# Kernel tuning notes

Hardware: AMD Instinct MI355X
Metric: run time of the kernel (lower is better)

The kernel has to match this reference:

```python
import jax, jax.numpy as jnp
import numpy as np

ALPHA = 13
B_POOL = 1.0
KERNEL = 2
STRIDE = 2
PADDING = 0


def _poly_eval(x, c):
    # Horner evaluation of sum_k c[k] * x**k (same math as power-basis sum)
    acc = jnp.zeros_like(x) + c[-1]
    for k in range(c.shape[0] - 2, -1, -1):
        acc = acc * x + c[k]
    return acc


def _sgn_approx(x, coeff_stages):
    # composed polynomial approximation of sign(x); B_relu = 1.0 so x/B == x
    for c in coeff_stages:
        x = _poly_eval(x, c)
    return x


def _max_approx(a, b, coeff_stages):
    d = a - b
    return (a + b + d * _sgn_approx(d, coeff_stages)) / 2.0


def setup_inputs() -> dict:
    key = jax.random.key(0)
    k1, k2, k3 = jax.random.split(key, 3)
    x = jax.random.uniform(k1, (32, 64, 112, 112), dtype=jnp.float32,
                           minval=-0.9, maxval=0.9)
    coeffs0 = 0.3 * jax.random.normal(k2, (8,), dtype=jnp.float32)
    coeffs1 = 0.3 * jax.random.normal(k3, (8,), dtype=jnp.float32)
    return {"x": x, "coeffs0": coeffs0, "coeffs1": coeffs1}


def reference(x, coeffs0, coeffs1):
    coeff_stages = (coeffs0, coeffs1)
    # zero padding (padding = 0 here, kept for generality)
    xp = jnp.pad(x, ((0, 0), (0, 0), (PADDING, PADDING), (PADDING, PADDING)))
    N, C, W, H = xp.shape
    i_num = (W - KERNEL) // STRIDE + 1  # 56
    j_num = (H - KERNEL) // STRIDE + 1  # 56
    # strided window extraction (im2col of the 2x2 pooling windows)
    ext = [xp[:, :, i:i + STRIDE * i_num:STRIDE, j:j + STRIDE * j_num:STRIDE]
           for i in range(KERNEL) for j in range(KERNEL)]
    # scale into the valid range of the sign approximation
    scaling_factor = (1.0 - 4.0 * 0.5 ** ALPHA) / (B_POOL * 2.0)
    ext = [e * scaling_factor + 0.5 for e in ext]
    # binary max tree via polynomial sign approximation
    s1 = _max_approx(ext[0], ext[1], coeff_stages)
    s2 = _max_approx(ext[2], ext[3], coeff_stages)
    res = _max_approx(s1, s2, coeff_stages)
    return ((res - 0.5) / scaling_factor).astype(jnp.float32)
```

## Files before the change

### kernel.cpp

```cpp
#include <hip/hip_runtime.h>


#define W_IN 112
#define W_OUT 56
#define CH_IN_STRIDE (112 * 112)
#define CH_OUT_STRIDE (56 * 56)

typedef float f4 __attribute__((ext_vector_type(4)));
typedef float f2 __attribute__((ext_vector_type(2)));

constexpr float SF     = 0.499755859375f;
constexpr float INV_SF = 4096.0f / 2047.0f;
constexpr float DCLAMP = 1.0e4f;

__device__ __forceinline__ float horner(float x, const float c[8]) {
    float acc = c[7];
#pragma unroll
    for (int k = 6; k >= 0; --k) acc = fmaf(acc, x, c[k]);
    return acc;
}

__device__ __forceinline__ float clampd(float x) {
    return fminf(fmaxf(x, -DCLAMP), DCLAMP);
}

__device__ __forceinline__ float max_leaf(float a, float b,
                                          const float c0[8], const float c1[8]) {
    float d = a - b;
    float s = horner(horner(d, c0), c1);
    return (a + b + d * s) * 0.5f;
}

__device__ __forceinline__ float max_root(float a, float b,
                                          const float c0[8], const float c1[8]) {
    float dc = clampd(a - b);
    float s  = horner(clampd(horner(dc, c0)), c1);
    return (a + b + dc * s) * 0.5f;
}

__device__ __forceinline__ float pool1(float e0, float e1, float e2, float e3,
                                       const float c0[8], const float c1[8]) {
    float p0 = fmaf(e0, SF, 0.5f);
    float p1 = fmaf(e1, SF, 0.5f);
    float p2 = fmaf(e2, SF, 0.5f);
    float p3 = fmaf(e3, SF, 0.5f);
    float s1 = max_leaf(p0, p1, c0, c1);
    float s2 = max_leaf(p2, p3, c0, c1);
    float r  = max_root(s1, s2, c0, c1);
    return (r - 0.5f) * INV_SF;
}

__global__ __launch_bounds__(256) void maxpool_approx_kernel(
    const float* __restrict__ x,
    const float* __restrict__ cc0,
    const float* __restrict__ cc1,
    float* __restrict__ out) {
    int t = blockIdx.x * blockDim.x + threadIdx.x;

    int j    = t % 28;
    int rest = t / 28;
    int r    = rest % 56;
    int nc   = rest / 56;

    float c0[8], c1[8];
#pragma unroll
    for (int k = 0; k < 8; ++k) { c0[k] = cc0[k]; c1[k] = cc1[k]; }

    const f4* base = (const f4*)(x + (size_t)nc * CH_IN_STRIDE
                                   + (size_t)(2 * r) * W_IN + 4 * j);
    const int rowf4 = W_IN / 4;

    f4 a = base[0];
    f4 b = base[rowf4];

    f2 res;
    res.x = pool1(a.x, a.y, b.x, b.y, c0, c1);
    res.y = pool1(a.z, a.w, b.z, b.w, c0, c1);

    f2* ob = (f2*)(out + (size_t)nc * CH_OUT_STRIDE + (size_t)r * W_OUT + 2 * j);
    *ob = res;
}

extern "C" void kernel_launch(void* const* d_in, const int* in_sizes, int n_in,
                              void* d_out, int out_size, void* d_ws, size_t ws_size,
                              hipStream_t stream) {
    const float* x   = (const float*)d_in[0];
    const float* cc0 = (const float*)d_in[1];
    const float* cc1 = (const float*)d_in[2];
    float* out = (float*)d_out;

    int total = 2048 * 56 * 28;
    int threads = 256;
    int blocks = total / threads;
    maxpool_approx_kernel<<<blocks, threads, 0, stream>>>(x, cc0, cc1, out);
}
```

Baseline: 154.5 us.

## Use persistent grid-stride loop with software prefetch of next inputs

Replaces the one-thread-per-task launch with a fixed grid of 2048 blocks that walk the work in a grid-stride loop. Each iteration loads the next task's two input rows before computing the current one, so global-memory latency overlaps with the polynomial arithmetic. Coefficient loads and launch overhead are amortised across iterations. The cost is extra registers for the prefetched vectors, fewer resident waves to hide latency, and possibly less even load balance.

```diff
diff --git a/kernel.cpp b/kernel.cpp
--- a/kernel.cpp
+++ b/kernel.cpp
@@ -5,6 +5,7 @@
 #define W_OUT 56
 #define CH_IN_STRIDE (112 * 112)
 #define CH_OUT_STRIDE (56 * 56)
+#define TOTAL_TASKS (2048 * 56 * 28)
 
 typedef float f4 __attribute__((ext_vector_type(4)));
 typedef float f2 __attribute__((ext_vector_type(2)));
@@ -50,35 +51,61 @@
     return (r - 0.5f) * INV_SF;
 }
 
-__global__ __launch_bounds__(256) void maxpool_approx_kernel(
+__device__ __forceinline__ const f4* in_addr(const float* x, int idx) {
+    int j    = idx % 28;
+    int rest = idx / 28;
+    int r    = rest % 56;
+    int nc   = rest / 56;
+    return (const f4*)(x + (size_t)nc * CH_IN_STRIDE
+                         + (size_t)(2 * r) * W_IN + 4 * j);
+}
+
+__device__ __forceinline__ f2* out_addr(float* out, int idx) {
+    int j    = idx % 28;
+    int rest = idx / 28;
+    int r    = rest % 56;
+    int nc   = rest / 56;
+    return (f2*)(out + (size_t)nc * CH_OUT_STRIDE + (size_t)r * W_OUT + 2 * j);
+}
+
+__global__ __launch_bounds__(256, 8) void maxpool_approx_kernel(
     const float* __restrict__ x,
     const float* __restrict__ cc0,
     const float* __restrict__ cc1,
     float* __restrict__ out) {
-    int t = blockIdx.x * blockDim.x + threadIdx.x;
-
-    int j    = t % 28;
-    int rest = t / 28;
-    int r    = rest % 56;
-    int nc   = rest / 56;
+    const int stride = gridDim.x * blockDim.x;
+    int idx = blockIdx.x * blockDim.x + threadIdx.x;
 
     float c0[8], c1[8];
 #pragma unroll
     for (int k = 0; k < 8; ++k) { c0[k] = cc0[k]; c1[k] = cc1[k]; }
 
-    const f4* base = (const f4*)(x + (size_t)nc * CH_IN_STRIDE
-                                   + (size_t)(2 * r) * W_IN + 4 * j);
     const int rowf4 = W_IN / 4;
 
-    f4 a = base[0];
-    f4 b = base[rowf4];
+    if (idx >= TOTAL_TASKS) return;
 
-    f2 res;
-    res.x = pool1(a.x, a.y, b.x, b.y, c0, c1);
-    res.y = pool1(a.z, a.w, b.z, b.w, c0, c1);
+    const f4* p = in_addr(x, idx);
+    f4 a = p[0];
+    f4 b = p[rowf4];
 
-    f2* ob = (f2*)(out + (size_t)nc * CH_OUT_STRIDE + (size_t)r * W_OUT + 2 * j);
-    *ob = res;
+    for (;;) {
+        int nidx = idx + stride;
+        f4 a2, b2;
+        bool have_next = (nidx < TOTAL_TASKS);
+        if (have_next) {
+            const f4* pn = in_addr(x, nidx);
+            a2 = pn[0];
+            b2 = pn[rowf4];
+        }
+
+        f2 res;
+        res.x = pool1(a.x, a.y, b.x, b.y, c0, c1);
+        res.y = pool1(a.z, a.w, b.z, b.w, c0, c1);
+        *out_addr(out, idx) = res;
+
+        if (!have_next) break;
+        a = a2; b = b2; idx = nidx;
+    }
 }
 
 extern "C" void kernel_launch(void* const* d_in, const int* in_sizes, int n_in,
@@ -89,8 +116,7 @@
     const float* cc1 = (const float*)d_in[2];
     float* out = (float*)d_out;
 
-    int total = 2048 * 56 * 28;
     int threads = 256;
-    int blocks = total / threads;
+    int blocks = 2048;
     maxpool_approx_kernel<<<blocks, threads, 0, stream>>>(x, cc0, cc1, out);
 }
```

New measurement: 156.6 us. Within noise of the previous version (+1.4%).
